# Kernel optimization log

Measured on AMD Instinct MI355X. Metric: run time of the kernel, lower is better.

## Reference

```python
import jax, jax.numpy as jnp
import numpy as np
from jax import lax

E = 4; D_MODEL = 128; D_FF = 128; DT_RANK = 32; D_STATE = 16
L = 12; PAD = 12  # padding_factor=1.0 -> pad L extra zeros
K_TOP = 6; U = 1e-6; EPS = 1e-5
BATCH = 8; NODES = 307; BN = BATCH * NODES
FREQ_IN = (L + PAD) // 2 + 1 + K_TOP  # 19
FREQ_OUT = L // 2 + 1                 # 7


def setup_inputs() -> dict:
    key = jax.random.key(0)
    ks = jax.random.split(key, 14)
    x = jax.random.normal(ks[0], (BN, L, D_MODEL), jnp.float32)
    graph = jax.random.normal(ks[1], (BATCH, L, D_FF, D_FF), jnp.float32) * (1.0 / D_FF)
    in_w = jax.random.normal(ks[2], (E, 2 * D_FF, D_MODEL), jnp.float32) * 0.05
    in_b = jax.random.normal(ks[3], (E, 2 * D_FF), jnp.float32) * 0.02
    x_w = jax.random.normal(ks[4], (E, DT_RANK + 2 * D_STATE + D_FF, D_FF), jnp.float32) * 0.05
    dt_w = jax.random.uniform(ks[5], (E, D_FF, DT_RANK), jnp.float32,
                              -(DT_RANK ** -0.5), DT_RANK ** -0.5)
    dt_b = -2.0 + 0.1 * jax.random.normal(ks[6], (E, D_FF), jnp.float32)
    A_log = jnp.broadcast_to(jnp.log(jnp.arange(1, D_STATE + 1, dtype=jnp.float32))[None, None, :],
                             (E, 1, D_STATE))
    out_w = jax.random.normal(ks[7], (E, D_MODEL, D_FF), jnp.float32) * 0.05
    out_b = jax.random.normal(ks[8], (E, D_MODEL), jnp.float32) * 0.02
    fw_r = jax.random.normal(ks[9], (E, FREQ_OUT, FREQ_IN), jnp.float32) * (FREQ_IN ** -0.5)
    fw_i = jax.random.normal(ks[10], (E, FREQ_OUT, FREQ_IN), jnp.float32) * (FREQ_IN ** -0.5)
    norm_w = jnp.ones((E, D_MODEL), jnp.float32)
    blk_w = jnp.full((E,), 0.5, jnp.float32)
    blk_b = jnp.full((E,), 0.5, jnp.float32)
    return dict(x=x, graph=graph, in_w=in_w, in_b=in_b, x_w=x_w, dt_w=dt_w, dt_b=dt_b,
                A_log=A_log, out_w=out_w, out_b=out_b, fw_r=fw_r, fw_i=fw_i,
                norm_w=norm_w, blk_w=blk_w, blk_b=blk_b)


def _rmsnorm(x, w):
    return x * lax.rsqrt(jnp.mean(x * x, axis=-1, keepdims=True) + EPS) * w


def _mamba_block(x, graph, in_w, in_b, x_w, dt_w, dt_b, A_log, out_w, out_b, fw_r, fw_i):
    bn, Ls, d = x.shape
    # --- FFT frequency gating ---
    x_padded = jnp.concatenate([x, jnp.zeros((bn, PAD, d), x.dtype)], axis=1)
    fp = jnp.fft.rfft(x_padded, axis=1)          # [bn, 13, d] complex
    f = jnp.fft.rfft(x, axis=1)                  # [bn, 7, d] complex
    sq_adj = (f.real + U) ** 2 + (f.imag + U) ** 2
    fs = -jnp.sort(-sq_adj, axis=1)[:, :K_TOP]   # top-K along freq dim, descending
    cat = jnp.concatenate([fp, fs.astype(fp.dtype)], axis=1)  # [bn, 19, d]
    W = lax.complex(fw_r, fw_i)                  # [7, 19]
    freq_proj = jnp.einsum('bkd,ok->bod', cat, W)  # [bn, 7, d]
    wf = jax.nn.softmax(freq_proj.real ** 2 + freq_proj.imag ** 2, axis=2)
    x_freq = jnp.fft.irfft(wf * f, axis=1)       # [bn, 12, d] (n = 2*(7-1))
    # --- input projection ---
    xz = x @ in_w.T + in_b
    xs, z = jnp.split(xz, 2, axis=-1)
    xs = jax.nn.silu(xs)
    # --- SSM ---
    A = -jnp.exp(A_log.astype(jnp.float32))      # [1, d_state]
    dbcd = xs @ x_w.T
    delta, B, C, Dp = jnp.split(dbcd, [DT_RANK, DT_RANK + D_STATE, DT_RANK + 2 * D_STATE], axis=-1)
    delta = jax.nn.softplus(delta @ dt_w.T + dt_b)  # [bn, L, d_ff]
    # graph mixing over nodes: bn = batch * n
    batch = graph.shape[0]
    delta = delta.reshape(batch, -1, Ls, D_FF)
    delta = jnp.einsum('bnsd,bsda->bnsa', delta, graph).reshape(bn, Ls, D_FF)
    deltaA = jnp.exp(delta[..., None] * A)             # [bn, L, d_ff, d_state]
    BX = delta[..., None] * B[:, :, None, :] * xs[..., None]
    dA_t = jnp.moveaxis(deltaA, 1, 0)
    bx_t = jnp.moveaxis(BX, 1, 0)

    def step(h, ab):
        dA, bx = ab
        h = dA * h + bx
        return h, h

    h0 = jnp.zeros((bn, D_FF, D_STATE), xs.dtype)
    _, hs = lax.scan(step, h0, (dA_t, bx_t))
    hs = jnp.moveaxis(hs, 0, 1)                        # [bn, L, d_ff, d_state]
    y = jnp.einsum('blds,bls->bld', hs, C) + Dp * xs
    # --- gate + output ---
    out = y * jax.nn.silu(z) * x_freq
    return out @ out_w.T + out_b


def reference(x, graph, in_w, in_b, x_w, dt_w, dt_b, A_log, out_w, out_b,
              fw_r, fw_i, norm_w, blk_w, blk_b):
    for i in range(E):
        xn = _rmsnorm(x, norm_w[i])
        out = _mamba_block(xn, graph, in_w[i], in_b[i], x_w[i], dt_w[i], dt_b[i],
                           A_log[i], out_w[i], out_b[i], fw_r[i], fw_i[i])
        out = blk_w[i] * out + blk_b[i]
        x = x + out  # dropout is identity in eval
    return jax.nn.silu(x)
```

## Files before the change

### kernel.cpp

```cpp
#include <hip/hip_runtime.h>
#include <math.h>

#define BN    2456
#define LSEQ  12
#define DM    128
#define NODES 307
#define MROWS 29472
#define FREQ_BLKS  1228
#define FUSED_BLKS 1920

typedef __bf16 bfx8 __attribute__((ext_vector_type(8)));
typedef __bf16 bfx4 __attribute__((ext_vector_type(4)));
typedef float  f32x4 __attribute__((ext_vector_type(4)));

#define MFMA16(a, b, c) __builtin_amdgcn_mfma_f32_16x16x32_bf16(a, b, c, 0, 0, 0)

__device__ __forceinline__ float fsilu(float v)     { return v / (1.0f + __expf(-v)); }
__device__ __forceinline__ float fsoftplus(float x) { return fmaxf(x, 0.f) + __logf(1.0f + __expf(-fabsf(x))); }

__global__ __launch_bounds__(256)
void k_convert(const float* __restrict__ in_w, const float* __restrict__ x_w,
               const float* __restrict__ dt_w, const float* __restrict__ out_w,
               const float* __restrict__ graph,
               const float* __restrict__ fw_r, const float* __restrict__ fw_i,
               __bf16* __restrict__ in_w_sw, __bf16* __restrict__ x_w_sw,
               __bf16* __restrict__ dtw_sw, __bf16* __restrict__ out_w_sw,
               __bf16* __restrict__ graph_sw, float* __restrict__ mw) {
    int idx = blockIdx.x * 256 + threadIdx.x;
    if (idx < 131072) {
        int o = idx;
        int e = o >> 15, r = o & 32767;
        int frag = r >> 9, lane = (r >> 3) & 63, j = r & 7;
        int nt = frag >> 2, kc = frag & 3, lm = lane & 15, lq = lane >> 4;
        in_w_sw[o] = (__bf16)in_w[e * 32768 + (nt * 16 + lm) * 128 + kc * 32 + lq * 8 + j];
        return;
    }
    idx -= 131072;
    if (idx < 98304) {
        int o = idx;
        int e = o / 24576, r = o - e * 24576;
        int frag = r >> 9, lane = (r >> 3) & 63, j = r & 7;
        int nt = frag >> 2, kc = frag & 3, lm = lane & 15, lq = lane >> 4;
        x_w_sw[o] = (__bf16)x_w[e * 24576 + (nt * 16 + lm) * 128 + kc * 32 + lq * 8 + j];
        return;
    }
    idx -= 98304;
    if (idx < 16384) {
        int o = idx;
        int e = o >> 12, r = o & 4095;
        int nt = r >> 9, lane = (r >> 3) & 63, j = r & 7;
        int lm = lane & 15, lq = lane >> 4;
        dtw_sw[o] = (__bf16)dt_w[e * 4096 + (nt * 16 + lm) * 32 + lq * 8 + j];
        return;
    }
    idx -= 16384;
    if (idx < 65536) {
        int o = idx;
        int e = o >> 14, r = o & 16383;
        int frag = r >> 9, lane = (r >> 3) & 63, j = r & 7;
        int f = frag >> 2, kc = frag & 3, lm = lane & 15, lq = lane >> 4;
        out_w_sw[o] = (__bf16)out_w[e * 16384 + (f * 16 + lm) * 128 + kc * 32 + lq * 8 + j];
        return;
    }
    idx -= 65536;
    if (idx < 1572864) {
        int bl = idx >> 14, r = idx & 16383;
        int dd = r >> 7, a = r & 127;
        int nt = a >> 4, lm = a & 15, kc = dd >> 5, lq = (dd >> 3) & 3, j = dd & 7;
        graph_sw[(size_t)bl * 16384 + ((size_t)((nt * 4 + kc) * 64 + lq * 16 + lm)) * 8 + j] =
            (__bf16)graph[(size_t)bl * 16384 + dd * 128 + a];
        return;
    }
    idx -= 1572864;
    if (idx < 336) {
        int o = idx;
        int e = o / 84, r = o - e * 84;
        int o2 = r / 12, l = r - o2 * 12;
        float mr = 0.f, mi = 0.f;
        for (int k = 0; k < 13; ++k) {
            float sv, cv;
            __sincosf(6.283185307179586f * (float)(k * l) / 24.0f, &sv, &cv);
            const float wr = fw_r[e * 133 + o2 * 19 + k], wi = fw_i[e * 133 + o2 * 19 + k];
            mr += wr * cv + wi * sv;
            mi += wi * cv - wr * sv;
        }
        mw[e * 256 + (o2 * 12 + l) * 2]     = mr;
        mw[e * 256 + (o2 * 12 + l) * 2 + 1] = mi;
        return;
    }
    idx -= 336;
    if (idx < 168) {
        int o = idx;
        int e = o / 42, r = o - e * 42;
        int o2 = r / 6, k = r - o2 * 6;
        mw[e * 256 + 168 + (o2 * 6 + k) * 2]     = fw_r[e * 133 + o2 * 19 + 13 + k];
        mw[e * 256 + 168 + (o2 * 6 + k) * 2 + 1] = fw_i[e * 133 + o2 * 19 + 13 + k];
    }
}

__global__ __launch_bounds__(256)
void k_fused(const float* __restrict__ xcur, const float* __restrict__ norm_w,
             const __bf16* __restrict__ WiSw, const float* __restrict__ in_b,
             const __bf16* __restrict__ WxSw, const __bf16* __restrict__ DWSw,
             const float* __restrict__ dt_b, const __bf16* __restrict__ GSw,
             const float* __restrict__ mw,
             __bf16* __restrict__ scanp, float* __restrict__ bcf32,
             __bf16* __restrict__ xfq_bf, int e) {
    const int tid = threadIdx.x;

    if (blockIdx.x < FREQ_BLKS) {
        __shared__ float sred2[2][2][12];
        const int hh = tid >> 7, t7 = tid & 127;
        const int lane = tid & 63, w2 = (tid >> 6) & 1;
        const int row = blockIdx.x * 2 + hh;
        const int b = row / NODES, n = row - b * NODES;

        constexpr float SQ32 = 0.8660254037844386f;
        constexpr float C12[12] = {1.f, SQ32, 0.5f, 0.f, -0.5f, -SQ32, -1.f, -SQ32, -0.5f, 0.f, 0.5f, SQ32};
        constexpr float S12[12] = {0.f, 0.5f, SQ32, 1.f, SQ32, 0.5f, 0.f, -0.5f, -SQ32, -1.f, -SQ32, -0.5f};

        const float* xp = xcur + (size_t)row * 1536 + t7;
        float xv[12], v[12];
#pragma unroll
        for (int l = 0; l < 12; ++l) { xv[l] = xp[l * 128]; v[l] = xv[l] * xv[l]; }
#pragma unroll
        for (int off = 32; off; off >>= 1)
#pragma unroll
            for (int i = 0; i < 12; ++i) v[i] += __shfl_xor(v[i], off, 64);
        if (lane == 0) {
#pragma unroll
            for (int i = 0; i < 12; ++i) sred2[hh][w2][i] = v[i];
        }
        __syncthreads();
#pragma unroll
        for (int i = 0; i < 12; ++i) v[i] = sred2[hh][0][i] + sred2[hh][1][i];
        __syncthreads();

        const float nrmw = norm_w[e * DM + t7];
        float xnr[12];
#pragma unroll
        for (int l = 0; l < 12; ++l)
            xnr[l] = xv[l] * rsqrtf(v[l] * (1.0f / 128.0f) + 1e-5f) * nrmw;

        float fr[7], fi[7];
#pragma unroll
        for (int o2 = 0; o2 < 7; ++o2) {
            float r = 0.f, im = 0.f;
#pragma unroll
            for (int l = 0; l < 12; ++l) {
                const int t = (o2 * l) % 12;
                r += xnr[l] * C12[t];
                im -= xnr[l] * S12[t];
            }
            fr[o2] = r; fi[o2] = im;
        }

        float a7[7];
#pragma unroll
        for (int o2 = 0; o2 < 7; ++o2) {
            const float ar = fr[o2] + 1e-6f, ai = fi[o2] + 1e-6f;
            a7[o2] = ar * ar + ai * ai;
        }
#pragma unroll
        for (int pss = 0; pss < 6; ++pss)
#pragma unroll
            for (int j = 0; j < 6; ++j) {
                const float hi = fmaxf(a7[j], a7[j + 1]);
                const float lo = fminf(a7[j], a7[j + 1]);
                a7[j] = hi; a7[j + 1] = lo;
            }

        const float* Me = mw + e * 256;
        float p7[7];
#pragma unroll
        for (int o2 = 0; o2 < 7; ++o2) {
            float pr = 0.f, pi = 0.f;
#pragma unroll
            for (int l = 0; l < 12; ++l) {
                pr += xnr[l] * Me[(o2 * 12 + l) * 2];
                pi += xnr[l] * Me[(o2 * 12 + l) * 2 + 1];
            }
#pragma unroll
            for (int k = 0; k < 6; ++k) {
                pr += a7[k] * Me[168 + (o2 * 6 + k) * 2];
                pi += a7[k] * Me[168 + (o2 * 6 + k) * 2 + 1];
            }
            p7[o2] = pr * pr + pi * pi;
        }

        float m7[7];
#pragma unroll
        for (int i = 0; i < 7; ++i) m7[i] = p7[i];
#pragma unroll
        for (int off = 32; off; off >>= 1)
#pragma unroll
            for (int i = 0; i < 7; ++i) m7[i] = fmaxf(m7[i], __shfl_xor(m7[i], off, 64));
        if (lane == 0) {
#pragma unroll
            for (int i = 0; i < 7; ++i) sred2[hh][w2][i] = m7[i];
        }
        __syncthreads();
#pragma unroll
        for (int i = 0; i < 7; ++i) m7[i] = fmaxf(sred2[hh][0][i], sred2[hh][1][i]);
        __syncthreads();

        float ex[7], sm[7];
#pragma unroll
        for (int i = 0; i < 7; ++i) { ex[i] = __expf(p7[i] - m7[i]); sm[i] = ex[i]; }
#pragma unroll
        for (int off = 32; off; off >>= 1)
#pragma unroll
            for (int i = 0; i < 7; ++i) sm[i] += __shfl_xor(sm[i], off, 64);
        if (lane == 0) {
#pragma unroll
            for (int i = 0; i < 7; ++i) sred2[hh][w2][i] = sm[i];
        }
        __syncthreads();
#pragma unroll
        for (int i = 0; i < 7; ++i) sm[i] = sred2[hh][0][i] + sred2[hh][1][i];

        float gr[7], gi[7];
#pragma unroll
        for (int o2 = 0; o2 < 7; ++o2) {
            const float wf = ex[o2] / sm[o2];
            gr[o2] = wf * fr[o2];
            gi[o2] = wf * fi[o2];
        }

        const size_t xb = ((size_t)(b * 12) * NODES + n) * 128 + t7;
#pragma unroll
        for (int l = 0; l < 12; ++l) {
            float val = gr[0] + ((l & 1) ? -gr[6] : gr[6]);
#pragma unroll
            for (int o2 = 1; o2 < 6; ++o2) {
                const int t = (o2 * l) % 12;
                val += 2.0f * (gr[o2] * C12[t] - gi[o2] * S12[t]);
            }
            xfq_bf[xb + (size_t)l * (NODES * 128)] = (__bf16)(val * (1.0f / 12.0f));
        }
        return;
    }

    __shared__ __bf16 sxs[16 * 136];
    __shared__ __bf16 sdelta[16 * 136];
    __shared__ __bf16 sdel32[16 * 40];
    __shared__ __align__(16) char sraw[16 * 520 * 2];
    float  (*sxf)[132]  = (float (*)[132])sraw;
    __bf16 (*sdump)[520] = (__bf16 (*)[520])sraw;

    const int bid = blockIdx.x - FREQ_BLKS;
    const int bl = bid / 20;
    const int n0 = (bid - bl * 20) * 16;
    const int wave = tid >> 6, lane = tid & 63;
    const int lm = lane & 15, lq = lane >> 4;
    const int b = bl / 12, l = bl - b * 12;
    const size_t rowbase = (size_t)bl * NODES + n0;

    for (int i = tid; i < 1024; i += 256) {
        const int node = i >> 6, dp2 = i & 63;
        const int gn = min(n0 + node, NODES - 1);
        *(float2*)(&sxf[node][dp2 * 2]) =
            *(const float2*)(xcur + ((size_t)(b * NODES + gn) * 12 + l) * 128 + dp2 * 2);
    }
    __syncthreads();

    float xv[4][8];
#pragma unroll
    for (int kc = 0; kc < 4; ++kc)
#pragma unroll
        for (int j = 0; j < 8; ++j) xv[kc][j] = sxf[lm][kc * 32 + lq * 8 + j];

    float ss = 0.f;
#pragma unroll
    for (int kc = 0; kc < 4; ++kc)
#pragma unroll
        for (int j = 0; j < 8; ++j) ss += xv[kc][j] * xv[kc][j];
    ss += __shfl_xor(ss, 16, 64);
    ss += __shfl_xor(ss, 32, 64);
    const float rms = rsqrtf(ss * (1.0f / 128.0f) + 1e-5f);

    bfx8 af[4];
    const float* nwp = norm_w + e * DM + lq * 8;
#pragma unroll
    for (int kc = 0; kc < 4; ++kc) {
        float4 w0 = *(const float4*)(nwp + kc * 32);
        float4 w1 = *(const float4*)(nwp + kc * 32 + 4);
        af[kc][0] = (__bf16)(xv[kc][0] * rms * w0.x);
        af[kc][1] = (__bf16)(xv[kc][1] * rms * w0.y);
        af[kc][2] = (__bf16)(xv[kc][2] * rms * w0.z);
        af[kc][3] = (__bf16)(xv[kc][3] * rms * w0.w);
        af[kc][4] = (__bf16)(xv[kc][4] * rms * w1.x);
        af[kc][5] = (__bf16)(xv[kc][5] * rms * w1.y);
        af[kc][6] = (__bf16)(xv[kc][6] * rms * w1.z);
        af[kc][7] = (__bf16)(xv[kc][7] * rms * w1.w);
    }
    __syncthreads();

    const __bf16* WxP = WxSw + (size_t)e * 24576;
    bfx8 b2[3][4];
#pragma unroll
    for (int ntl = 0; ntl < 3; ++ntl)
#pragma unroll
        for (int kc = 0; kc < 4; ++kc)
            b2[ntl][kc] = *(const bfx8*)(WxP + (((wave * 3 + ntl) * 4 + kc) * 64 + lane) * 8);

    const __bf16* WiP = WiSw + (size_t)e * 32768;
    f32x4 acc[4];
#pragma unroll
    for (int nt = 0; nt < 4; ++nt) acc[nt] = (f32x4){0.f, 0.f, 0.f, 0.f};
#pragma unroll
    for (int ntl = 0; ntl < 4; ++ntl) {
        const int nt = wave * 4 + ntl;
#pragma unroll
        for (int kc = 0; kc < 4; ++kc) {
            bfx8 bb = *(const bfx8*)(WiP + ((nt * 4 + kc) * 64 + lane) * 8);
            acc[ntl] = MFMA16(af[kc], bb, acc[ntl]);
        }
    }

    const __bf16* DWp = DWSw + (size_t)e * 4096;
    bfx8 b3[2];
#pragma unroll
    for (int ntl = 0; ntl < 2; ++ntl)
        b3[ntl] = *(const bfx8*)(DWp + ((wave * 2 + ntl) * 64 + lane) * 8);
    const __bf16* Gp = GSw + (size_t)bl * 16384;
    bfx8 b4[2][4];
#pragma unroll
    for (int ntl = 0; ntl < 2; ++ntl)
#pragma unroll
        for (int kc = 0; kc < 4; ++kc)
            b4[ntl][kc] = *(const bfx8*)(Gp + (((wave * 2 + ntl) * 4 + kc) * 64 + lane) * 8);

#pragma unroll
    for (int ntl = 0; ntl < 4; ++ntl) {
        const int col = wave * 64 + ntl * 16 + lm;
        const float bias = in_b[e * 256 + col];
#pragma unroll
        for (int r = 0; r < 4; ++r) {
            const int node = lq * 4 + r;
            const float v = fsilu(acc[ntl][r] + bias);
            if (col < 128) {
                sxs[node * 136 + col] = (__bf16)v;
                sdump[node][col * 4 + 1] = (__bf16)v;
            } else {
                sdump[node][(col - 128) * 4 + 3] = (__bf16)v;
            }
        }
    }
    __syncthreads();

    bfx8 ax[4];
#pragma unroll
    for (int kc = 0; kc < 4; ++kc)
        ax[kc] = *(const bfx8*)(sxs + lm * 136 + kc * 32 + lq * 8);

    f32x4 xacc[3];
#pragma unroll
    for (int nt = 0; nt < 3; ++nt) xacc[nt] = (f32x4){0.f, 0.f, 0.f, 0.f};
#pragma unroll
    for (int ntl = 0; ntl < 3; ++ntl)
#pragma unroll
        for (int kc = 0; kc < 4; ++kc)
            xacc[ntl] = MFMA16(ax[kc], b2[ntl][kc], xacc[ntl]);

#pragma unroll
    for (int ntl = 0; ntl < 3; ++ntl) {
        const int col = (wave * 3 + ntl) * 16 + lm;
#pragma unroll
        for (int r = 0; r < 4; ++r) {
            const int node = lq * 4 + r;
            const float v = xacc[ntl][r];
            if (col < 32) sdel32[node * 40 + col] = (__bf16)v;
            else if (col < 64) { if ((n0 + node) < NODES) bcf32[(rowbase + node) * 32 + (col - 32)] = v; }
            else sdump[node][(col - 64) * 4 + 2] = (__bf16)v;
        }
    }
    __syncthreads();

    bfx8 ad = *(const bfx8*)(sdel32 + lm * 40 + lq * 8);
    const f32x4 z4 = {0.f, 0.f, 0.f, 0.f};
#pragma unroll
    for (int ntl = 0; ntl < 2; ++ntl) {
        f32x4 dacc = MFMA16(ad, b3[ntl], z4);
        const int col = (wave * 2 + ntl) * 16 + lm;
        const float bias = dt_b[e * 128 + col];
#pragma unroll
        for (int r = 0; r < 4; ++r) {
            const int node = lq * 4 + r;
            sdelta[node * 136 + col] = (__bf16)fsoftplus(dacc[r] + bias);
        }
    }
    __syncthreads();

    bfx8 ag[4];
#pragma unroll
    for (int kc = 0; kc < 4; ++kc)
        ag[kc] = *(const bfx8*)(sdelta + lm * 136 + kc * 32 + lq * 8);

#pragma unroll
    for (int ntl = 0; ntl < 2; ++ntl) {
        f32x4 gacc = z4;
#pragma unroll
        for (int kc = 0; kc < 4; ++kc)
            gacc = MFMA16(ag[kc], b4[ntl][kc], gacc);
        const int col = (wave * 2 + ntl) * 16 + lm;
#pragma unroll
        for (int r = 0; r < 4; ++r) {
            const int node = lq * 4 + r;
            sdump[node][col * 4 + 0] = (__bf16)gacc[r];
        }
    }
    __syncthreads();

    __bf16* dst = scanp + rowbase * 512;
#pragma unroll
    for (int k = 0; k < 4; ++k) {
        const int c = k * 256 + tid;
        const int node = c >> 6;
        if ((n0 + node) < NODES)
            *(bfx8*)(dst + (size_t)c * 8) = *(const bfx8*)(&sdump[node][(c & 63) * 8]);
    }
}

__global__ __launch_bounds__(128)
void k_scanout(const float* __restrict__ xcur, const __bf16* __restrict__ scanp,
               const float* __restrict__ bcf32, const __bf16* __restrict__ xfq_bf,
               const float* __restrict__ A_log, const __bf16* __restrict__ WoSw,
               const float* __restrict__ out_b, const float* __restrict__ blk_w,
               const float* __restrict__ blk_b, float* __restrict__ xout, int e, int last) {
    __shared__ __bf16 s_out[16 * 136];
    const int row = blockIdx.x, tid = threadIdx.x;
    const int b = row / NODES, n = row - b * NODES;

    constexpr float LOGT[16] = {0.f, 0.6931472f, 1.0986123f, 1.3862944f, 1.6094379f, 1.7917595f,
                                1.9459101f, 2.0794415f, 2.1972246f, 2.3025851f, 2.3978953f,
                                2.4849066f, 2.5649494f, 2.6390573f, 2.7080502f, 2.7725887f};

    bfx4 sc12[12];
    const size_t sb = ((size_t)(b * 12) * NODES + n) * 512 + (size_t)tid * 4;
#pragma unroll
    for (int l = 0; l < 12; ++l)
        sc12[l] = *(const bfx4*)(scanp + sb + (size_t)l * (NODES * 512));

    __bf16 xq[12];
    const size_t xb = ((size_t)(b * 12) * NODES + n) * 128 + tid;
#pragma unroll
    for (int l = 0; l < 12; ++l)
        xq[l] = xfq_bf[xb + (size_t)l * (NODES * 128)];

    int chainOK = 1;
#pragma unroll
    for (int s = 0; s < 16; ++s)
        chainOK &= (fabsf(A_log[e * 16 + s] - LOGT[s]) < 1e-4f) ? 1 : 0;

#pragma unroll
    for (int r = 12; r < 16; ++r) s_out[r * 136 + tid] = (__bf16)0.f;

    float h[16];
#pragma unroll
    for (int j = 0; j < 16; ++j) h[j] = 0.f;

    if (chainOK) {
        float q1a[12];
#pragma unroll
        for (int l = 0; l < 12; ++l) q1a[l] = __expf(-(float)sc12[l][0]);
#pragma unroll
        for (int l = 0; l < 12; ++l) {
            const float dl = (float)sc12[l][0], xsv = (float)sc12[l][1];
            const float dlx = dl * xsv;
            const float* bc = bcf32 + ((size_t)(b * 12 + l) * NODES + n) * 32;
            const float q1 = q1a[l];
            const float q2 = q1 * q1, q4 = q2 * q2, q8 = q4 * q4;
            float pw[16];
            pw[0] = q1;        pw[1] = q2;        pw[2] = q1 * q2;    pw[3] = q4;
            pw[4] = q1 * q4;   pw[5] = q2 * q4;   pw[6] = pw[2] * q4; pw[7] = q8;
            pw[8] = q1 * q8;   pw[9] = q2 * q8;   pw[10] = pw[2] * q8; pw[11] = q4 * q8;
            pw[12] = pw[4] * q8; pw[13] = pw[5] * q8; pw[14] = pw[6] * q8; pw[15] = q8 * q8;
            float y0 = 0.f, y1 = 0.f, y2 = 0.f, y3 = 0.f;
#pragma unroll
            for (int j = 0; j < 4; ++j) {
                h[j]      = pw[j]      * h[j]      + bc[j]      * dlx;  y0 += h[j]      * bc[16 + j];
                h[j + 4]  = pw[j + 4]  * h[j + 4]  + bc[j + 4]  * dlx;  y1 += h[j + 4]  * bc[20 + j];
                h[j + 8]  = pw[j + 8]  * h[j + 8]  + bc[j + 8]  * dlx;  y2 += h[j + 8]  * bc[24 + j];
                h[j + 12] = pw[j + 12] * h[j + 12] + bc[j + 12] * dlx;  y3 += h[j + 12] * bc[28 + j];
            }
            float y = (y0 + y1) + (y2 + y3);
            y += (float)sc12[l][2] * xsv;
            const float g = y * (float)sc12[l][3] * (float)xq[l];
            s_out[l * 136 + tid] = (__bf16)g;
        }
    } else {
        float As[16];
#pragma unroll
        for (int s = 0; s < 16; ++s) As[s] = -__expf(A_log[e * 16 + s]);
#pragma unroll
        for (int l = 0; l < 12; ++l) {
            const float dl = (float)sc12[l][0], xsv = (float)sc12[l][1];
            const float dlx = dl * xsv;
            const float* bc = bcf32 + ((size_t)(b * 12 + l) * NODES + n) * 32;
            float y = 0.f;
#pragma unroll
            for (int j = 0; j < 16; ++j) {
                const float a = __expf(dl * As[j]);
                h[j] = a * h[j] + bc[j] * dlx;
                y += h[j] * bc[16 + j];
            }
            y += (float)sc12[l][2] * xsv;
            const float g = y * (float)sc12[l][3] * (float)xq[l];
            s_out[l * 136 + tid] = (__bf16)g;
        }
    }
    __syncthreads();

    const int wave = tid >> 6, lane = tid & 63;
    const int lm = lane & 15, lq = lane >> 4;
    const __bf16* Wop = WoSw + (size_t)e * 16384;
    bfx8 a[4];
#pragma unroll
    for (int kc = 0; kc < 4; ++kc)
        a[kc] = *(const bfx8*)(s_out + lm * 136 + kc * 32 + lq * 8);

    f32x4 acc[4];
#pragma unroll
    for (int nt = 0; nt < 4; ++nt) acc[nt] = (f32x4){0.f, 0.f, 0.f, 0.f};
#pragma unroll
    for (int nt = 0; nt < 4; ++nt) {
        const int f = wave * 4 + nt;
#pragma unroll
        for (int kc = 0; kc < 4; ++kc) {
            bfx8 bb = *(const bfx8*)(Wop + ((f * 4 + kc) * 64 + lane) * 8);
            acc[nt] = MFMA16(a[kc], bb, acc[nt]);
        }
    }

    const float bw = blk_w[e], bb2 = blk_b[e];
#pragma unroll
    for (int nt = 0; nt < 4; ++nt) {
        const int col = wave * 64 + nt * 16 + lm;
        const float ob = out_b[e * 128 + col];
#pragma unroll
        for (int r = 0; r < 4; ++r) {
            const int m = lq * 4 + r;
            if (m < 12) {
                const size_t gi = (size_t)row * 1536 + m * 128 + col;
                float vv = bw * (acc[nt][r] + ob) + bb2 + xcur[gi];
                if (last) vv = fsilu(vv);
                xout[gi] = vv;
            }
        }
    }
}

extern "C" void kernel_launch(void* const* d_in, const int* in_sizes, int n_in,
                              void* d_out, int out_size, void* d_ws, size_t ws_size,
                              hipStream_t stream) {
    (void)in_sizes; (void)n_in; (void)out_size; (void)ws_size;
    const float* x_in   = (const float*)d_in[0];
    const float* graph  = (const float*)d_in[1];
    const float* in_w   = (const float*)d_in[2];
    const float* in_b   = (const float*)d_in[3];
    const float* x_w    = (const float*)d_in[4];
    const float* dt_w   = (const float*)d_in[5];
    const float* dt_b   = (const float*)d_in[6];
    const float* A_log  = (const float*)d_in[7];
    const float* out_w  = (const float*)d_in[8];
    const float* out_b  = (const float*)d_in[9];
    const float* fw_r   = (const float*)d_in[10];
    const float* fw_i   = (const float*)d_in[11];
    const float* norm_w = (const float*)d_in[12];
    const float* blk_w  = (const float*)d_in[13];
    const float* blk_b  = (const float*)d_in[14];
    float* out = (float*)d_out;

    float* ws = (float*)d_ws;
    size_t o = 0;
    __bf16* in_w_sw  = (__bf16*)(ws + o); o += 131072 / 2;
    __bf16* x_w_sw   = (__bf16*)(ws + o); o += 98304 / 2;
    __bf16* dtw_sw   = (__bf16*)(ws + o); o += 16384 / 2;
    __bf16* out_w_sw = (__bf16*)(ws + o); o += 65536 / 2;
    __bf16* graph_sw = (__bf16*)(ws + o); o += 1572864 / 2;
    const size_t NE = (size_t)MROWS * 128;
    __bf16* scanp    = (__bf16*)(ws + o); o += (size_t)MROWS * 512 / 2;
    __bf16* xfq_bf   = (__bf16*)(ws + o); o += NE / 2;
    float*  bcf32    = ws + o;            o += (size_t)MROWS * 32;
    float*  mw       = ws + o;            o += 1024;

    hipLaunchKernelGGL(k_convert, dim3(7362), dim3(256), 0, stream,
                       in_w, x_w, dt_w, out_w, graph, fw_r, fw_i,
                       in_w_sw, x_w_sw, dtw_sw, out_w_sw, graph_sw, mw);

    for (int e = 0; e < 4; ++e) {
        const float* xcur = (e == 0) ? x_in : (const float*)out;
        const int last = (e == 3) ? 1 : 0;
        hipLaunchKernelGGL(k_fused, dim3(FREQ_BLKS + FUSED_BLKS), dim3(256), 0, stream,
                           xcur, norm_w, in_w_sw, in_b, x_w_sw, dtw_sw, dt_b, graph_sw,
                           mw, scanp, bcf32, xfq_bf, e);
        hipLaunchKernelGGL(k_scanout, dim3(BN), dim3(128), 0, stream,
                           xcur, scanp, bcf32, xfq_bf, A_log,
                           out_w_sw, out_b, blk_w, blk_b, out, e, last);
    }
}
```

Measured before the change: 377.5 us.

## Interleave freq and fused blocks; drop LDS staging for x and scanp output

```diff
diff --git a/kernel.cpp b/kernel.cpp
--- a/kernel.cpp
+++ b/kernel.cpp
@@ -107,12 +107,16 @@
              __bf16* __restrict__ scanp, float* __restrict__ bcf32,
              __bf16* __restrict__ xfq_bf, int e) {
     const int tid = threadIdx.x;
-
-    if (blockIdx.x < FREQ_BLKS) {
+    const int bid0 = blockIdx.x;
+    int isFreq, wid;
+    if (bid0 < 2 * FREQ_BLKS) { isFreq = !(bid0 & 1); wid = bid0 >> 1; }
+    else                      { isFreq = 0; wid = FREQ_BLKS + (bid0 - 2 * FREQ_BLKS); }
+
+    if (isFreq) {
         __shared__ float sred2[2][2][12];
         const int hh = tid >> 7, t7 = tid & 127;
         const int lane = tid & 63, w2 = (tid >> 6) & 1;
-        const int row = blockIdx.x * 2 + hh;
+        const int row = wid * 2 + hh;
         const int b = row / NODES, n = row - b * NODES;
 
         constexpr float SQ32 = 0.8660254037844386f;
@@ -244,32 +248,24 @@
     __shared__ __bf16 sxs[16 * 136];
     __shared__ __bf16 sdelta[16 * 136];
     __shared__ __bf16 sdel32[16 * 40];
-    __shared__ __align__(16) char sraw[16 * 520 * 2];
-    float  (*sxf)[132]  = (float (*)[132])sraw;
-    __bf16 (*sdump)[520] = (__bf16 (*)[520])sraw;
-
-    const int bid = blockIdx.x - FREQ_BLKS;
-    const int bl = bid / 20;
-    const int n0 = (bid - bl * 20) * 16;
+
+    const int bl = wid / 20;
+    const int n0 = (wid - bl * 20) * 16;
     const int wave = tid >> 6, lane = tid & 63;
     const int lm = lane & 15, lq = lane >> 4;
     const int b = bl / 12, l = bl - b * 12;
     const size_t rowbase = (size_t)bl * NODES + n0;
 
-    for (int i = tid; i < 1024; i += 256) {
-        const int node = i >> 6, dp2 = i & 63;
-        const int gn = min(n0 + node, NODES - 1);
-        *(float2*)(&sxf[node][dp2 * 2]) =
-            *(const float2*)(xcur + ((size_t)(b * NODES + gn) * 12 + l) * 128 + dp2 * 2);
-    }
-    __syncthreads();
-
+    const int nodeA = min(n0 + lm, NODES - 1);
+    const float* xrow = xcur + ((size_t)(b * NODES + nodeA) * 12 + l) * 128 + lq * 8;
     float xv[4][8];
 #pragma unroll
-    for (int kc = 0; kc < 4; ++kc)
-#pragma unroll
-        for (int j = 0; j < 8; ++j) xv[kc][j] = sxf[lm][kc * 32 + lq * 8 + j];
-
+    for (int kc = 0; kc < 4; ++kc) {
+        float4 p0 = *(const float4*)(xrow + kc * 32);
+        float4 p1 = *(const float4*)(xrow + kc * 32 + 4);
+        xv[kc][0] = p0.x; xv[kc][1] = p0.y; xv[kc][2] = p0.z; xv[kc][3] = p0.w;
+        xv[kc][4] = p1.x; xv[kc][5] = p1.y; xv[kc][6] = p1.z; xv[kc][7] = p1.w;
+    }
     float ss = 0.f;
 #pragma unroll
     for (int kc = 0; kc < 4; ++kc)
@@ -294,7 +290,6 @@
         af[kc][6] = (__bf16)(xv[kc][6] * rms * w1.z);
         af[kc][7] = (__bf16)(xv[kc][7] * rms * w1.w);
     }
-    __syncthreads();
 
     const __bf16* WxP = WxSw + (size_t)e * 24576;
     bfx8 b2[3][4];
@@ -339,11 +334,12 @@
         for (int r = 0; r < 4; ++r) {
             const int node = lq * 4 + r;
             const float v = fsilu(acc[ntl][r] + bias);
+            const int ok = (n0 + node) < NODES;
             if (col < 128) {
                 sxs[node * 136 + col] = (__bf16)v;
-                sdump[node][col * 4 + 1] = (__bf16)v;
-            } else {
-                sdump[node][(col - 128) * 4 + 3] = (__bf16)v;
+                if (ok) scanp[(rowbase + node) * 512 + col * 4 + 1] = (__bf16)v;
+            } else if (ok) {
+                scanp[(rowbase + node) * 512 + (col - 128) * 4 + 3] = (__bf16)v;
             }
         }
     }
@@ -370,9 +366,10 @@
         for (int r = 0; r < 4; ++r) {
             const int node = lq * 4 + r;
             const float v = xacc[ntl][r];
+            const int ok = (n0 + node) < NODES;
             if (col < 32) sdel32[node * 40 + col] = (__bf16)v;
-            else if (col < 64) { if ((n0 + node) < NODES) bcf32[(rowbase + node) * 32 + (col - 32)] = v; }
-            else sdump[node][(col - 64) * 4 + 2] = (__bf16)v;
+            else if (col < 64) { if (ok) bcf32[(rowbase + node) * 32 + (col - 32)] = v; }
+            else if (ok) scanp[(rowbase + node) * 512 + (col - 64) * 4 + 2] = (__bf16)v;
         }
     }
     __syncthreads();
@@ -407,18 +404,9 @@
 #pragma unroll
         for (int r = 0; r < 4; ++r) {
             const int node = lq * 4 + r;
-            sdump[node][col * 4 + 0] = (__bf16)gacc[r];
-        }
-    }
-    __syncthreads();
-
-    __bf16* dst = scanp + rowbase * 512;
-#pragma unroll
-    for (int k = 0; k < 4; ++k) {
-        const int c = k * 256 + tid;
-        const int node = c >> 6;
-        if ((n0 + node) < NODES)
-            *(bfx8*)(dst + (size_t)c * 8) = *(const bfx8*)(&sdump[node][(c & 63) * 8]);
+            if ((n0 + node) < NODES)
+                scanp[(rowbase + node) * 512 + col * 4 + 0] = (__bf16)gacc[r];
+        }
     }
 }
 
@@ -592,7 +580,7 @@
     for (int e = 0; e < 4; ++e) {
         const float* xcur = (e == 0) ? x_in : (const float*)out;
         const int last = (e == 3) ? 1 : 0;
-        hipLaunchKernelGGL(k_fused, dim3(FREQ_BLKS + FUSED_BLKS), dim3(256), 0, stream,
+        hipLaunchKernelGGL(k_fused, dim3(2 * FREQ_BLKS + (FUSED_BLKS - FREQ_BLKS)), dim3(256), 0, stream,
                            xcur, norm_w, in_w_sw, in_b, x_w_sw, dtw_sw, dt_b, graph_sw,
                            mw, scanp, bcf32, xfq_bf, e);
         hipLaunchKernelGGL(k_scanout, dim3(BN), dim3(128), 0, stream,
```

Measured after the change: 447.6 us. 1.19x slower.
